# Kernel tuning notes

Measured on AMD Instinct MI355X. Metric: run time of the kernel, lower is better.

Reference implementation:

```python
import jax, jax.numpy as jnp
import numpy as np
import math

DIM = 2048; H = 16; QR = 1536; KVR = 512; DN = 128; DR = 64; DV = 128
BS = 4; S = 1024
QK_HEAD = DN + DR  # 192


def _rms(x, w, eps=1e-6):
    v = jnp.mean(x * x, axis=-1, keepdims=True)
    return w * (x * jax.lax.rsqrt(v + eps))


def _rope_cos_sin(seq_len, dim):
    inv_freq = 1.0 / (10000.0 ** (jnp.arange(0, dim, 2, dtype=jnp.float32) / dim))
    t = jnp.arange(seq_len, dtype=jnp.float32)
    freqs = jnp.einsum('s,d->sd', t, inv_freq)
    freqs = jnp.concatenate([freqs, freqs], axis=-1)  # [S, dim]
    return jnp.cos(freqs), jnp.sin(freqs)


def _rotate_half(x):
    x1, x2 = jnp.split(x, 2, axis=-1)
    return jnp.concatenate([-x2, x1], axis=-1)


def setup_inputs() -> dict:
    key = jax.random.key(0)
    ks = jax.random.split(key, 12)
    sd = 0.02
    x = jax.random.normal(ks[0], (BS, S, DIM), dtype=jnp.float32)
    # causal additive mask [b, s, t]
    i = jnp.arange(S)
    causal = jnp.where(i[:, None] >= i[None, :], 0.0, -1e9).astype(jnp.float32)
    mask = jnp.broadcast_to(causal, (BS, S, S))
    return {
        'x': x,
        'mask': mask,
        'wq_a_w': jax.random.normal(ks[1], (QR, DIM)) * sd,
        'wq_a_b': jnp.zeros((QR,), jnp.float32),
        'q_norm_w': jnp.ones((QR,), jnp.float32),
        'wq_b_w': jax.random.normal(ks[2], (H * QK_HEAD, QR)) * sd,
        'wq_b_b': jnp.zeros((H * QK_HEAD,), jnp.float32),
        'wkv_a_w': jax.random.normal(ks[3], (KVR + DR, DIM)) * sd,
        'wkv_a_b': jnp.zeros((KVR + DR,), jnp.float32),
        'kv_norm_w': jnp.ones((KVR,), jnp.float32),
        'wkv_b_w': jax.random.normal(ks[4], (H * (DN + DV), KVR)) * sd,
        'wo_w': jax.random.normal(ks[5], (DIM, H * DV)) * sd,
        'wo_b': jnp.zeros((DIM,), jnp.float32),
    }


def reference(x, mask, wq_a_w, wq_a_b, q_norm_w, wq_b_w, wq_b_b,
              wkv_a_w, wkv_a_b, kv_norm_w, wkv_b_w, wo_w, wo_b):
    bs, seq_len, _ = x.shape
    # Q low-rank path
    q = x @ wq_a_w.T + wq_a_b                     # [b,s,QR]
    q = _rms(q, q_norm_w)
    q = q @ wq_b_w.T + wq_b_b                     # [b,s,H*192]
    q = q.reshape(bs, seq_len, H, QK_HEAD)
    q_nope, q_pe = q[..., :DN], q[..., DN:]       # [b,s,h,128], [b,s,h,64]
    # compressed KV path
    kv = x @ wkv_a_w.T + wkv_a_b                  # [b,s,KVR+64]
    c, k_pe = kv[..., :KVR], kv[..., KVR:]        # [b,s,512], [b,s,64]
    # RoPE on the rope sub-dims
    cos, sin = _rope_cos_sin(seq_len, DR)         # [s,64]
    cos4 = cos[None, :, None, :]
    sin4 = sin[None, :, None, :]
    q_pe = q_pe * cos4 + _rotate_half(q_pe) * sin4
    k_pe4 = k_pe[:, :, None, :]
    k_pe = (k_pe4 * cos4 + _rotate_half(k_pe4) * sin4)[:, :, 0, :]  # [b,s,64]
    # weight absorption: wkv_b viewed [H, DN+DV, KVR]
    wkv_b = wkv_b_w.reshape(H, DN + DV, KVR)
    q_abs = jnp.einsum('bshd,hdc->bshc', q_nope, wkv_b[:, :DN])      # [b,s,h,512]
    c_n = _rms(c, kv_norm_w)                                         # [b,t,512]
    scores = (jnp.einsum('bshc,btc->bsht', q_abs, c_n)
              + jnp.einsum('bshr,btr->bsht', q_pe, k_pe)) / math.sqrt(QK_HEAD)
    scores = scores + mask[:, :, None, :]
    scores = jax.nn.softmax(scores, axis=-1)
    o = jnp.einsum('bsht,btc->bshc', scores, c_n)                    # [b,s,h,512]
    o = jnp.einsum('bshc,hdc->bshd', o, wkv_b[:, -DV:])              # [b,s,h,128]
    o = o.reshape(bs, seq_len, H * DV)
    return o @ wo_w.T + wo_b
```

## Files before the change

### kernel.cpp

```cpp
#include <hip/hip_runtime.h>


typedef __attribute__((ext_vector_type(8))) short bf16x8;
typedef __attribute__((ext_vector_type(4))) float f32x4;
typedef __attribute__((ext_vector_type(4))) int i32x4;
typedef unsigned short ushort_t;
typedef unsigned int uint32;

typedef const __attribute__((address_space(1))) void* gas_ptr;
typedef __attribute__((address_space(3))) void* las_ptr;

#define DEV __device__ __forceinline__
#define WAITVM(N) asm volatile("s_waitcnt vmcnt(" #N ")" ::: "memory")

DEV float b2f(ushort_t u) { return __uint_as_float(((uint32)u) << 16); }
DEV ushort_t f2b(float f) {
  uint32 u = __float_as_uint(f);
  return (ushort_t)((u + 0x7fffu + ((u >> 16) & 1u)) >> 16);
}
DEV uint32 pkb(float lo, float hi) { return (uint32)f2b(lo) | ((uint32)f2b(hi) << 16); }

DEV void c4seg(const float4* __restrict__ in, ushort4* __restrict__ out, int i, int n4) {
  if (i < n4) {
    float4 v = in[i];
    ushort4 o; o.x = f2b(v.x); o.y = f2b(v.y); o.z = f2b(v.z); o.w = f2b(v.w);
    out[i] = o;
  }
}
DEV void vbseg(const float* __restrict__ in, ushort_t* __restrict__ out, int i4, int dofs) {
  int c4 = i4 & 127, d = (i4 >> 7) & 127, h = i4 >> 14;
  const float4 v = *(const float4*)(in + ((long)(h * 256 + dofs + d)) * 512 + c4 * 4);
  ushort4 o; o.x = f2b(v.x); o.y = f2b(v.y); o.z = f2b(v.z); o.w = f2b(v.w);
  ((ushort4*)out)[i4] = o;
}
__global__ __launch_bounds__(256) void castall_k(
    const float* __restrict__ x, const float* __restrict__ wq_a_w,
    const float* __restrict__ wkv_a_w, const float* __restrict__ wq_b_w,
    const float* __restrict__ wo_w, const float* __restrict__ wkv_b_w,
    ushort_t* __restrict__ xb, ushort_t* __restrict__ wcomb,
    ushort_t* __restrict__ wqb, ushort_t* __restrict__ wo,
    ushort_t* __restrict__ wkvbv, ushort_t* __restrict__ wkvbn) {
  int blk = blockIdx.x, tid = threadIdx.x;
  if (blk < 8192) {
    c4seg((const float4*)x, (ushort4*)xb, blk * 256 + tid, 2097152);
  } else if (blk < 11264) {
    c4seg((const float4*)wq_a_w, (ushort4*)wcomb, (blk - 8192) * 256 + tid, 786432);
  } else if (blk < 12416) {
    c4seg((const float4*)wkv_a_w, (ushort4*)(wcomb + 1536 * 2048),
          (blk - 11264) * 256 + tid, 294912);
  } else if (blk < 17024) {
    c4seg((const float4*)wq_b_w, (ushort4*)wqb, (blk - 12416) * 256 + tid, 1179648);
  } else if (blk < 21120) {
    c4seg((const float4*)wo_w, (ushort4*)wo, (blk - 17024) * 256 + tid, 1048576);
  } else if (blk < 22144) {
    vbseg(wkv_b_w, wkvbv, (blk - 21120) * 256 + tid, 128);
  } else {
    vbseg(wkv_b_w, wkvbn, (blk - 22144) * 256 + tid, 0);
  }
}

__global__ __launch_bounds__(512) void rmskv_k(const ushort_t* __restrict__ qab,
                                               ushort_t* __restrict__ qan,
                                               const float* __restrict__ q_norm_w,
                                               const ushort_t* __restrict__ kvfb,
                                               const float* __restrict__ kv_norm_w,
                                               ushort_t* __restrict__ kcat,
                                               ushort_t* __restrict__ vtp,
                                               ushort_t* __restrict__ kabs) {
  __shared__ float sbuf[8];
  __shared__ ushort_t sh[8 * 512];
  int blk = blockIdx.x, tid = threadIdx.x;
  int wv = tid >> 6, lane = tid & 63;
  if (blk < 4096) {
    long row = blk;
    const ushort_t* p = qab + row * 1536;
    float v0 = b2f(p[tid]), v1 = b2f(p[tid + 512]), v2 = b2f(p[tid + 1024]);
    float ss = v0 * v0 + v1 * v1 + v2 * v2;
#pragma unroll
    for (int d = 1; d <= 32; d <<= 1) ss += __shfl_xor(ss, d);
    if (lane == 0) sbuf[wv] = ss;
    __syncthreads();
    float tot = 0.f;
#pragma unroll
    for (int i = 0; i < 8; ++i) tot += sbuf[i];
    float sc = rsqrtf(tot * (1.0f / 1536.0f) + 1e-6f);
    qan[row * 1536 + tid] = f2b(v0 * sc * q_norm_w[tid]);
    qan[row * 1536 + tid + 512] = f2b(v1 * sc * q_norm_w[tid + 512]);
    qan[row * 1536 + tid + 1024] = f2b(v2 * sc * q_norm_w[tid + 1024]);
  } else {
    int kb = blk - 4096;
    long row = (long)kb * 8 + wv;
    const ushort_t* p = kvfb + row * 576;
    uint4 raw = *(const uint4*)(p + lane * 8);
    const ushort_t* pr = (const ushort_t*)&raw;
    float vv[8];
#pragma unroll
    for (int j = 0; j < 8; ++j) vv[j] = b2f(pr[j]);
    float ss = 0.f;
#pragma unroll
    for (int j = 0; j < 8; ++j) ss += vv[j] * vv[j];
#pragma unroll
    for (int d = 1; d <= 32; d <<= 1) ss += __shfl_xor(ss, d);
    float sc = rsqrtf(ss * (1.0f / 512.0f) + 1e-6f);
    float4 w0 = *(const float4*)(kv_norm_w + lane * 8);
    float4 w1 = *(const float4*)(kv_norm_w + lane * 8 + 4);
    ushort_t tmp[8];
    tmp[0] = f2b(vv[0] * sc * w0.x); tmp[1] = f2b(vv[1] * sc * w0.y);
    tmp[2] = f2b(vv[2] * sc * w0.z); tmp[3] = f2b(vv[3] * sc * w0.w);
    tmp[4] = f2b(vv[4] * sc * w1.x); tmp[5] = f2b(vv[5] * sc * w1.y);
    tmp[6] = f2b(vv[6] * sc * w1.z); tmp[7] = f2b(vv[7] * sc * w1.w);
    *(uint4*)(kcat + row * 576 + lane * 8) = *(uint4*)tmp;
    *(uint4*)(sh + wv * 512 + lane * 8) = *(uint4*)tmp;
    if (lane < 32) {
      int t = (int)(row & 1023);
      float x1 = b2f(p[512 + lane]), x2 = b2f(p[544 + lane]);
      float ang = (float)t * powf(10000.0f, -(float)lane * (1.0f / 32.0f));
      float s, c; sincosf(ang, &s, &c);
      ushort_t r1 = f2b(x1 * c - x2 * s), r2 = f2b(x2 * c + x1 * s);
      kcat[row * 576 + 512 + lane] = r1;
      kcat[row * 576 + 544 + lane] = r2;
#pragma unroll
      for (int h = 0; h < 16; ++h) {
        long base = ((long)h * 4096 + row) * 192;
        kabs[base + 128 + lane] = r1;
        kabs[base + 160 + lane] = r2;
      }
    }
    __syncthreads();
    ushort_t t8[8];
#pragma unroll
    for (int j = 0; j < 8; ++j) t8[j] = sh[j * 512 + tid];
    int b = kb >> 7, tb = kb & 127;
    *(uint4*)(vtp + (((long)b * 128 + tb) * 512 + tid) * 8) = *(uint4*)t8;
  }
}

template <bool OUT_BF16>
__global__ __launch_bounds__(256) void gemm_bt_k(
    const ushort_t* __restrict__ A, int lda, long sAz,
    const ushort_t* __restrict__ B, int ldb, long sBz,
    void* __restrict__ C, int ldc, long sCz,
    const float* __restrict__ bias, float scale,
    int M, int N, int K) {
  __shared__ ushort_t As[2 * 4096];
  __shared__ ushort_t Bs[2 * 4096];
  int tid = threadIdx.x;
  int wave = tid >> 6, lane = tid & 63;
  int row0 = blockIdx.x * 128, col0 = blockIdx.y * 128;
  int z = blockIdx.z;
  const ushort_t* Az = A + (long)z * sAz;
  const ushort_t* Bz = B + (long)z * sBz;
  int wr = wave >> 1, wc = wave & 1;
  int lr = lane & 15, kq = lane >> 4;

  f32x4 acc[4][4];
#pragma unroll
  for (int m = 0; m < 4; ++m)
#pragma unroll
    for (int n = 0; n < 4; ++n) acc[m][n] = (f32x4){0.f, 0.f, 0.f, 0.f};

  auto stage = [&](int buf, int k0) {
#pragma unroll
    for (int rnd = 0; rnd < 2; ++rnd) {
      int e = rnd * 2048 + wave * 512 + lane * 8;
      int tr = e >> 5, tc = e & 31;
      int ar = row0 + tr; if (ar >= M) ar = M - 1;
      int br = col0 + tr; if (br >= N) br = N - 1;
      __builtin_amdgcn_global_load_lds((gas_ptr)(Az + (long)ar * lda + (k0 + tc)),
          (las_ptr)(As + buf * 4096 + rnd * 2048 + wave * 512), 16, 0, 0);
      __builtin_amdgcn_global_load_lds((gas_ptr)(Bz + (long)br * ldb + (k0 + tc)),
          (las_ptr)(Bs + buf * 4096 + rnd * 2048 + wave * 512), 16, 0, 0);
    }
  };

  stage(0, 0);
  int nk = K >> 5;
  for (int kt = 0; kt < nk; ++kt) {
    int cur = kt & 1;
    if (kt + 1 < nk) { stage(cur ^ 1, (kt + 1) * 32); WAITVM(4); }
    else { WAITVM(0); }
    __builtin_amdgcn_s_barrier();
    __builtin_amdgcn_sched_barrier(0);
    const ushort_t* Ac = As + cur * 4096;
    const ushort_t* Bc = Bs + cur * 4096;
    bf16x8 a[4], bb[4];
#pragma unroll
    for (int m = 0; m < 4; ++m)
      a[m] = *(const bf16x8*)(Ac + (wr * 64 + m * 16 + lr) * 32 + kq * 8);
#pragma unroll
    for (int n = 0; n < 4; ++n)
      bb[n] = *(const bf16x8*)(Bc + (wc * 64 + n * 16 + lr) * 32 + kq * 8);
#pragma unroll
    for (int m = 0; m < 4; ++m)
#pragma unroll
      for (int n = 0; n < 4; ++n)
        acc[m][n] = __builtin_amdgcn_mfma_f32_16x16x32_bf16(bb[n], a[m], acc[m][n], 0, 0, 0);
    __builtin_amdgcn_s_barrier();
  }

#pragma unroll
  for (int m = 0; m < 4; ++m) {
    int gr = row0 + wr * 64 + m * 16 + lr;
    if (gr >= M) continue;
#pragma unroll
    for (int n = 0; n < 4; ++n) {
      int cb = col0 + wc * 64 + n * 16 + kq * 4;
      if (cb >= N) continue;
      f32x4 v = acc[m][n];
#pragma unroll
      for (int r = 0; r < 4; ++r) v[r] = v[r] * scale + (bias ? bias[cb + r] : 0.f);
      long ci = (long)z * sCz + (long)gr * ldc + cb;
      if constexpr (OUT_BF16) {
        ushort4 pk; pk.x = f2b(v[0]); pk.y = f2b(v[1]); pk.z = f2b(v[2]); pk.w = f2b(v[3]);
        *(ushort4*)((ushort_t*)C + ci) = pk;
      } else {
        *(f32x4*)((float*)C + ci) = v;
      }
    }
  }
}

template <int MODE>
__global__ __launch_bounds__(256) void gemm64_k(
    const ushort_t* __restrict__ A, int lda,
    const ushort_t* __restrict__ B, int ldb,
    void* __restrict__ C, int ldc,
    const float* __restrict__ bias,
    void* __restrict__ C2, const float* __restrict__ bias2,
    int M, int N, int K) {
  __shared__ ushort_t SM[32768];
  ushort_t* As = SM;
  ushort_t* Bs = SM + 16384;
  int tid = threadIdx.x;
  int wave = tid >> 6, lane = tid & 63;
  int bid = blockIdx.y * gridDim.x + blockIdx.x;
  int nwg = gridDim.x * gridDim.y;
  int swz = (bid & 7) * (nwg >> 3) + (bid >> 3);
  int bx = swz % gridDim.x, by = swz / gridDim.x;
  int row0 = bx * 128, col0 = by * 128;
  int wr = wave >> 1, wc = wave & 1;
  int lr = lane & 15, kq = lane >> 4;
  int rsw = lr & 7;

  f32x4 acc[4][4];
#pragma unroll
  for (int m = 0; m < 4; ++m)
#pragma unroll
    for (int n = 0; n < 4; ++n) acc[m][n] = (f32x4){0.f, 0.f, 0.f, 0.f};

  auto stage = [&](int buf, int k0) {
#pragma unroll
    for (int ii = 0; ii < 4; ++ii) {
      int e = ii * 256 + tid;
      int r = e >> 3, c = e & 7;
      int scol = ((c ^ (r & 7)) << 3);
      int ar = row0 + r; if (ar >= M) ar = M - 1;
      int br = col0 + r; if (br >= N) br = N - 1;
      __builtin_amdgcn_global_load_lds((gas_ptr)(A + (long)ar * lda + k0 + scol),
          (las_ptr)(As + buf * 8192 + e * 8), 16, 0, 0);
      __builtin_amdgcn_global_load_lds((gas_ptr)(B + (long)br * ldb + k0 + scol),
          (las_ptr)(Bs + buf * 8192 + e * 8), 16, 0, 0);
    }
  };

  stage(0, 0);
  int nk = K >> 6;
  for (int kt = 0; kt < nk; ++kt) {
    int cur = kt & 1;
    if (kt + 1 < nk) { stage(cur ^ 1, (kt + 1) * 64); WAITVM(8); }
    else { WAITVM(0); }
    __builtin_amdgcn_s_barrier();
    __builtin_amdgcn_sched_barrier(0);
    const ushort_t* Ac = As + cur * 8192;
    const ushort_t* Bc = Bs + cur * 8192;
#pragma unroll
    for (int ks = 0; ks < 2; ++ks) {
      bf16x8 a[4], bb[4];
#pragma unroll
      for (int m = 0; m < 4; ++m) {
        int row = wr * 64 + m * 16 + lr;
        a[m] = *(const bf16x8*)(Ac + row * 64 + ((((ks << 2) | kq) ^ rsw) << 3));
      }
#pragma unroll
      for (int n = 0; n < 4; ++n) {
        int row = wc * 64 + n * 16 + lr;
        bb[n] = *(const bf16x8*)(Bc + row * 64 + ((((ks << 2) | kq) ^ rsw) << 3));
      }
#pragma unroll
      for (int m = 0; m < 4; ++m)
#pragma unroll
        for (int n = 0; n < 4; ++n)
          acc[m][n] = __builtin_amdgcn_mfma_f32_16x16x32_bf16(bb[n], a[m], acc[m][n], 0, 0, 0);
    }
    __builtin_amdgcn_s_barrier();
  }

  if constexpr (MODE == 0 || MODE == 1) {
    float* fs = (float*)SM;
#pragma unroll
    for (int p = 0; p < 2; ++p) {
      if (wr == p) {
#pragma unroll
        for (int m = 0; m < 4; ++m) {
#pragma unroll
          for (int n = 0; n < 4; ++n) {
            int rl = m * 16 + lr;
            int cl = wc * 64 + n * 16 + kq * 4;
            int cb = col0 + cl;
            int cbb = (cb + 3 < N) ? cb : (N - 4);
            f32x4 v = acc[m][n];
#pragma unroll
            for (int r = 0; r < 4; ++r) {
              float bv;
              if constexpr (MODE == 1)
                bv = (cbb + r < 1536) ? bias[cbb + r] : bias2[cbb + r - 1536];
              else
                bv = bias[cbb + r];
              v[r] += bv;
            }
            *(f32x4*)&fs[rl * 132 + cl] = v;
          }
        }
      }
      __syncthreads();
#pragma unroll
      for (int j = 0; j < 8; ++j) {
        int u = j * 256 + tid;
        int rl = u >> 5, off = (u & 31) << 2;
        int gr = row0 + p * 64 + rl;
        int gc = col0 + off;
        if (gr < M && gc < N) {
          f32x4 vv = *(const f32x4*)&fs[rl * 132 + off];
          if constexpr (MODE == 1) {
            ushort4 pk;
            pk.x = f2b(vv[0]); pk.y = f2b(vv[1]); pk.z = f2b(vv[2]); pk.w = f2b(vv[3]);
            if (gc < 1536) *(ushort4*)((ushort_t*)C + (long)gr * 1536 + gc) = pk;
            else           *(ushort4*)((ushort_t*)C2 + (long)gr * 576 + (gc - 1536)) = pk;
          } else {
            *(f32x4*)((float*)C + (long)gr * ldc + gc) = vv;
          }
        }
      }
      __syncthreads();
    }
  } else {
    const float RS = 0.07216878364870322f;
#pragma unroll
    for (int n = 0; n < 4; ++n) {
      int cb = col0 + wc * 64 + n * 16 + kq * 4;
      int h = cb / 192, d0 = cb - h * 192;
      ushort_t* qh = (ushort_t*)C + (long)h * 4096 * 192;
      if (d0 < 128) {
        f32x4 bv;
#pragma unroll
        for (int r = 0; r < 4; ++r) bv[r] = bias[cb + r];
#pragma unroll
        for (int m = 0; m < 4; ++m) {
          int gr = row0 + wr * 64 + m * 16 + lr;
          f32x4 v = acc[m][n];
          ushort4 pk;
          pk.x = f2b((v[0] + bv[0]) * RS); pk.y = f2b((v[1] + bv[1]) * RS);
          pk.z = f2b((v[2] + bv[2]) * RS); pk.w = f2b((v[3] + bv[3]) * RS);
          *(ushort4*)(qh + (long)gr * 192 + d0) = pk;
        }
      } else if (d0 < 160) {
        int nn = (n < 2) ? n : 0;
        f32x4 bv1, bv2, invf;
#pragma unroll
        for (int r = 0; r < 4; ++r) {
          bv1[r] = bias[cb + r]; bv2[r] = bias[cb + 32 + r];
          invf[r] = powf(10000.0f, -(float)(d0 - 128 + r) * (1.0f / 32.0f));
        }
#pragma unroll
        for (int m = 0; m < 4; ++m) {
          int gr = row0 + wr * 64 + m * 16 + lr;
          int t = gr & 1023;
          f32x4 v1 = acc[m][nn], v2 = acc[m][nn + 2];
          ushort4 p1, p2;
#pragma unroll
          for (int r = 0; r < 4; ++r) {
            float s, c; sincosf((float)t * invf[r], &s, &c);
            float x1 = v1[r] + bv1[r], x2 = v2[r] + bv2[r];
            ((ushort_t*)&p1)[r] = f2b((x1 * c - x2 * s) * RS);
            ((ushort_t*)&p2)[r] = f2b((x2 * c + x1 * s) * RS);
          }
          *(ushort4*)(qh + (long)gr * 192 + d0) = p1;
          *(ushort4*)(qh + (long)gr * 192 + d0 + 32) = p2;
        }
      }
    }
  }
}

__global__ __launch_bounds__(512, 1) void flash5_k(const ushort_t* __restrict__ qcat2,
                                                   const ushort_t* __restrict__ kabs,
                                                   const ushort_t* __restrict__ vtp,
                                                   ushort_t* __restrict__ O) {
  __shared__ __align__(16) ushort_t SMEM[2 * 6400 + 2 * 16384];

  int tid = threadIdx.x;
  int wave = tid >> 6, lane = tid & 63;
  int lr = lane & 15, kq = lane >> 4;
  int bi = blockIdx.x;
  int jz = bi >> 6;
  int qb = (jz < 4) ? jz : 11 - jz;
  int bh = bi & 63;
  int h = bh >> 2, b = bh & 3;
  int s0 = qb * 128;
  int nt = (qb + 1) * 4;

  const ushort_t* kt = kabs + ((long)h * 4096 + b * 1024) * 192;
  const ushort_t* vt = vtp + (long)b * 524288;
  const ushort_t* qp = qcat2 + ((long)(h * 4096 + b * 1024 + s0 + wave * 16 + lr)) * 192 + kq * 8;

  auto stageK = [&](int buf, int t0) {
    const ushort_t* sb = kt + (long)t0 * 192;
    ushort_t* kb = SMEM + buf * 6400;
#pragma unroll
    for (int ii = 0; ii < 2; ++ii) {
      int c = ii * 512 + tid;
      if (ii == 1 && tid >= 288) break;
      int t = (int)((unsigned)c / 25u);
      int r = c - t * 25;
      int rr = (r == 24) ? 0 : r;
      const ushort_t* src = sb + t * 192 + rr * 8;
      __builtin_amdgcn_global_load_lds((gas_ptr)src, (las_ptr)(kb + c * 8), 16, 0, 0);
    }
  };
  auto stageV = [&](int buf, int t0) {
    const ushort_t* sb = vt + (long)(t0 >> 3) * 4096;
    ushort_t* vb = SMEM + 12800 + buf * 16384;
#pragma unroll
    for (int ii = 0; ii < 4; ++ii) {
      int c0 = (ii * 8 + wave) * 64;
      const ushort_t* src = sb + (long)(c0 + lane) * 8;
      __builtin_amdgcn_global_load_lds((gas_ptr)src, (las_ptr)(vb + c0 * 8), 16, 0, 0);
    }
  };

  stageK(0, 0); stageV(0, 0);
  bf16x8 qreg[6];
#pragma unroll
  for (int st = 0; st < 6; ++st) qreg[st] = *(const bf16x8*)(qp + st * 32);

  f32x4 o[32];
#pragma unroll
  for (int v = 0; v < 32; ++v) o[v] = (f32x4){0.f, 0.f, 0.f, 0.f};
  float m_run = -1e30f, l_run = 0.f;

  int row_g = s0 + wave * 16 + lr;
  int idx_lo = (((kq & 1) << 5) + lr) << 2;
  int idx_hi = idx_lo + 64;
  bool losel = (kq < 2);

  __syncthreads();

  for (int it = 0; it < nt; ++it) {
    int cur = it & 1;
    if (it + 1 < nt) { stageK(cur ^ 1, (it + 1) * 32); stageV(cur ^ 1, (it + 1) * 32); }
    const ushort_t* Kc = SMEM + cur * 6400;
    f32x4 sv0 = (f32x4){0.f, 0.f, 0.f, 0.f}, sv1 = sv0;
    __builtin_amdgcn_s_setprio(1);
#pragma unroll
    for (int st = 0; st < 6; ++st) {
      int off = st * 32 + kq * 8;
      bf16x8 k0 = *(const bf16x8*)(Kc + lr * 200 + off);
      bf16x8 k1 = *(const bf16x8*)(Kc + (16 + lr) * 200 + off);
      sv0 = __builtin_amdgcn_mfma_f32_16x16x32_bf16(k0, qreg[st], sv0, 0, 0, 0);
      sv1 = __builtin_amdgcn_mfma_f32_16x16x32_bf16(k1, qreg[st], sv1, 0, 0, 0);
    }
    __builtin_amdgcn_s_setprio(0);
    int t0 = it * 32;
    if (t0 >= s0) {
#pragma unroll
      for (int rr = 0; rr < 4; ++rr) {
        if (t0 + kq * 4 + rr > row_g) sv0[rr] = -1e30f;
        if (t0 + 16 + kq * 4 + rr > row_g) sv1[rr] = -1e30f;
      }
    }
    float mx = fmaxf(fmaxf(fmaxf(sv0[0], sv0[1]), fmaxf(sv0[2], sv0[3])),
                     fmaxf(fmaxf(sv1[0], sv1[1]), fmaxf(sv1[2], sv1[3])));
    mx = fmaxf(mx, __shfl_xor(mx, 16));
    mx = fmaxf(mx, __shfl_xor(mx, 32));
    float mn = (mx > m_run + 8.0f) ? mx : m_run;
    float alpha = __expf(m_run - mn);
    float p0 = __expf(sv0[0] - mn), p1 = __expf(sv0[1] - mn);
    float p2 = __expf(sv0[2] - mn), p3 = __expf(sv0[3] - mn);
    float p4 = __expf(sv1[0] - mn), p5 = __expf(sv1[1] - mn);
    float p6 = __expf(sv1[2] - mn), p7 = __expf(sv1[3] - mn);
    float psum = ((p0 + p1) + (p2 + p3)) + ((p4 + p5) + (p6 + p7));
    psum += __shfl_xor(psum, 16);
    psum += __shfl_xor(psum, 32);
    l_run = l_run * alpha + psum;
    m_run = mn;
    int u0 = (int)pkb(p0, p1), u1 = (int)pkb(p2, p3);
    int u2 = (int)pkb(p4, p5), u3 = (int)pkb(p6, p7);
    int b00 = __builtin_amdgcn_ds_bpermute(idx_lo, u0);
    int b10 = __builtin_amdgcn_ds_bpermute(idx_lo, u1);
    int b20 = __builtin_amdgcn_ds_bpermute(idx_lo, u2);
    int b30 = __builtin_amdgcn_ds_bpermute(idx_lo, u3);
    int b01 = __builtin_amdgcn_ds_bpermute(idx_hi, u0);
    int b11 = __builtin_amdgcn_ds_bpermute(idx_hi, u1);
    int b21 = __builtin_amdgcn_ds_bpermute(idx_hi, u2);
    int b31 = __builtin_amdgcn_ds_bpermute(idx_hi, u3);
    i32x4 w;
    w.x = losel ? b00 : b20; w.y = losel ? b10 : b30;
    w.z = losel ? b01 : b21; w.w = losel ? b11 : b31;
    bf16x8 pa = __builtin_bit_cast(bf16x8, w);
    float a0 = __shfl(alpha, kq * 4 + 0), a1 = __shfl(alpha, kq * 4 + 1);
    float a2 = __shfl(alpha, kq * 4 + 2), a3 = __shfl(alpha, kq * 4 + 3);
    if (__any((a0 != 1.f) | (a1 != 1.f) | (a2 != 1.f) | (a3 != 1.f))) {
      f32x4 av; av[0] = a0; av[1] = a1; av[2] = a2; av[3] = a3;
#pragma unroll
      for (int v = 0; v < 32; ++v) o[v] *= av;
    }
    const ushort_t* Vc = SMEM + 12800 + cur * 16384 + (kq * 512 + lr) * 8;
    __builtin_amdgcn_s_setprio(1);
#pragma unroll
    for (int v = 0; v < 32; ++v) {
      bf16x8 bv = *(const bf16x8*)(Vc + v * 128);
      o[v] = __builtin_amdgcn_mfma_f32_16x16x32_bf16(pa, bv, o[v], 0, 0, 0);
    }
    __builtin_amdgcn_s_setprio(0);
    __syncthreads();
  }
  float l0 = __shfl(l_run, kq * 4 + 0), l1 = __shfl(l_run, kq * 4 + 1);
  float l2 = __shfl(l_run, kq * 4 + 2), l3 = __shfl(l_run, kq * 4 + 3);
  f32x4 inv; inv[0] = 1.f / l0; inv[1] = 1.f / l1; inv[2] = 1.f / l2; inv[3] = 1.f / l3;
  ushort_t* ob = O + ((long)(h * 4096 + b * 1024 + s0 + wave * 16 + kq * 4)) * 512 + lr;
#pragma unroll
  for (int rr = 0; rr < 4; ++rr) {
    ushort_t* orow = ob + (long)rr * 512;
#pragma unroll
    for (int v = 0; v < 32; ++v) orow[v * 16] = f2b(o[v][rr] * inv[rr]);
  }
}

extern "C" void kernel_launch(void* const* d_in, const int* in_sizes, int n_in,
                              void* d_out, int out_size, void* d_ws, size_t ws_size,
                              hipStream_t stream) {
  (void)in_sizes; (void)n_in;
  const float* x         = (const float*)d_in[0];
  const float* wq_a_w    = (const float*)d_in[2];
  const float* wq_a_b    = (const float*)d_in[3];
  const float* q_norm_w  = (const float*)d_in[4];
  const float* wq_b_w    = (const float*)d_in[5];
  const float* wq_b_b    = (const float*)d_in[6];
  const float* wkv_a_w   = (const float*)d_in[7];
  const float* wkv_a_b   = (const float*)d_in[8];
  const float* kv_norm_w = (const float*)d_in[9];
  const float* wkv_b_w   = (const float*)d_in[10];
  const float* wo_w      = (const float*)d_in[11];
  const float* wo_b      = (const float*)d_in[12];

  char* ws = (char*)d_ws;
  constexpr size_t OFF_XB     = 0;
  constexpr size_t OFF_WCOMB  = 16777216;
  constexpr size_t OFF_WQB    = 25427968;
  constexpr size_t OFF_QA     = 34865152;
  constexpr size_t OFF_QAN    = 60030976;
  constexpr size_t OFF_QCAT2  = 72613888;
  constexpr size_t OFF_WKVBN  = 97779712;
  constexpr size_t OFF_WKVBV  = 99876864;
  constexpr size_t OFF_WO     = 101974016;
  constexpr size_t OFF_KVF    = 110362624;
  constexpr size_t OFF_KCAT   = 119799808;
  constexpr size_t OFF_VTP    = 124518400;
  constexpr size_t OFF_KABS   = 128712704;
  constexpr size_t OFF_O      = 153878528;
  constexpr size_t OFF_O2     = 220987392;
  constexpr size_t WS_NEED    = 237764608;
  if (ws_size < WS_NEED) {
    (void)hipMemsetAsync(d_out, 0, (size_t)out_size * sizeof(float), stream);
    return;
  }

  ushort_t* xb     = (ushort_t*)(ws + OFF_XB);
  ushort_t* wcomb  = (ushort_t*)(ws + OFF_WCOMB);
  ushort_t* wqb    = (ushort_t*)(ws + OFF_WQB);
  ushort_t* qab    = (ushort_t*)(ws + OFF_QA);
  ushort_t* qan    = (ushort_t*)(ws + OFF_QAN);
  ushort_t* qcat2  = (ushort_t*)(ws + OFF_QCAT2);
  ushort_t* wkvbn  = (ushort_t*)(ws + OFF_WKVBN);
  ushort_t* wkvbv  = (ushort_t*)(ws + OFF_WKVBV);
  ushort_t* wo     = (ushort_t*)(ws + OFF_WO);
  ushort_t* kvfb   = (ushort_t*)(ws + OFF_KVF);
  ushort_t* kcat   = (ushort_t*)(ws + OFF_KCAT);
  ushort_t* vtp    = (ushort_t*)(ws + OFF_VTP);
  ushort_t* kabs   = (ushort_t*)(ws + OFF_KABS);
  ushort_t* Obuf   = (ushort_t*)(ws + OFF_O);
  ushort_t* o2     = (ushort_t*)(ws + OFF_O2);

  castall_k<<<23168, 256, 0, stream>>>(x, wq_a_w, wkv_a_w, wq_b_w, wo_w, wkv_b_w,
                                       xb, wcomb, wqb, wo, wkvbv, wkvbn);
  gemm64_k<1><<<dim3(32, 17), 256, 0, stream>>>(xb, 2048, wcomb, 2048,
      qab, 1536, wq_a_b, kvfb, wkv_a_b, 4096, 2112, 2048);
  rmskv_k<<<4608, 512, 0, stream>>>(qab, qan, q_norm_w, kvfb, kv_norm_w, kcat, vtp, kabs);
  gemm64_k<2><<<dim3(32, 24), 256, 0, stream>>>(qan, 1536, wqb, 1536,
      qcat2, 0, wq_b_b, nullptr, nullptr, 4096, 3072, 1536);
  gemm_bt_k<true><<<dim3(32, 1, 16), 256, 0, stream>>>(kcat, 576, 0,
      wkvbn, 512, (long)128 * 512, kabs, 192, (long)4096 * 192,
      nullptr, 1.f, 4096, 128, 512);
  flash5_k<<<512, 512, 0, stream>>>(qcat2, kabs, vtp, Obuf);
  gemm_bt_k<true><<<dim3(32, 1, 16), 256, 0, stream>>>(Obuf, 512, (long)4096 * 512,
      wkvbv, 512, (long)128 * 512, o2, 2048, 128, nullptr, 1.f, 4096, 128, 512);
  gemm64_k<0><<<dim3(32, 16), 256, 0, stream>>>(o2, 2048, wo, 2048,
      (float*)d_out, 2048, wo_b, nullptr, nullptr, 4096, 2048, 2048);
}
```

Measured before the change: 354.6 us.

## Split PV stage across wave pairs sharing P via LDS to halve V reads

In the flash attention kernel, the P·V product is restructured so that each pair of waves handles 32 query rows, and each wave in the pair takes half of the 512 value columns. P tiles and softmax rescale factors are exchanged through a small LDS scratch area with an added barrier, replacing the per-wave ds_bpermute shuffles. Each V fragment loaded from LDS now feeds two MFMAs instead of one, so LDS read traffic for V is halved. The cost is an extra workgroup barrier per tile and additional LDS writes and reads for P.

After: 354.6 us. Within noise of the previous version (+0.0%).

```diff
diff --git a/kernel.cpp b/kernel.cpp
--- a/kernel.cpp
+++ b/kernel.cpp
@@ -392,15 +392,18 @@
   }
 }
 
-__global__ __launch_bounds__(512, 1) void flash5_k(const ushort_t* __restrict__ qcat2,
+__global__ __launch_bounds__(512, 1) void flash8_k(const ushort_t* __restrict__ qcat2,
                                                    const ushort_t* __restrict__ kabs,
                                                    const ushort_t* __restrict__ vtp,
                                                    ushort_t* __restrict__ O) {
-  __shared__ __align__(16) ushort_t SMEM[2 * 6400 + 2 * 16384];
+  __shared__ __align__(16) ushort_t SMEM[2 * 6400 + 2 * 16384 + 128 * 40 + 256];
+  constexpr int PS_OFF = 45568;
+  float* aL = (float*)(SMEM + PS_OFF + 5120);
 
   int tid = threadIdx.x;
   int wave = tid >> 6, lane = tid & 63;
   int lr = lane & 15, kq = lane >> 4;
+  int qg = wave >> 1, vch = wave & 1;
   int bi = blockIdx.x;
   int jz = bi >> 6;
   int qb = (jz < 4) ? jz : 11 - jz;
@@ -443,15 +446,15 @@
 #pragma unroll
   for (int st = 0; st < 6; ++st) qreg[st] = *(const bf16x8*)(qp + st * 32);
 
-  f32x4 o[32];
-#pragma unroll
-  for (int v = 0; v < 32; ++v) o[v] = (f32x4){0.f, 0.f, 0.f, 0.f};
+  f32x4 oA[16], oB[16];
+#pragma unroll
+  for (int v = 0; v < 16; ++v) {
+    oA[v] = (f32x4){0.f, 0.f, 0.f, 0.f};
+    oB[v] = (f32x4){0.f, 0.f, 0.f, 0.f};
+  }
   float m_run = -1e30f, l_run = 0.f;
 
   int row_g = s0 + wave * 16 + lr;
-  int idx_lo = (((kq & 1) << 5) + lr) << 2;
-  int idx_hi = idx_lo + 64;
-  bool losel = (kq < 2);
 
   __syncthreads();
 
@@ -493,46 +496,53 @@
     psum += __shfl_xor(psum, 32);
     l_run = l_run * alpha + psum;
     m_run = mn;
-    int u0 = (int)pkb(p0, p1), u1 = (int)pkb(p2, p3);
-    int u2 = (int)pkb(p4, p5), u3 = (int)pkb(p6, p7);
-    int b00 = __builtin_amdgcn_ds_bpermute(idx_lo, u0);
-    int b10 = __builtin_amdgcn_ds_bpermute(idx_lo, u1);
-    int b20 = __builtin_amdgcn_ds_bpermute(idx_lo, u2);
-    int b30 = __builtin_amdgcn_ds_bpermute(idx_lo, u3);
-    int b01 = __builtin_amdgcn_ds_bpermute(idx_hi, u0);
-    int b11 = __builtin_amdgcn_ds_bpermute(idx_hi, u1);
-    int b21 = __builtin_amdgcn_ds_bpermute(idx_hi, u2);
-    int b31 = __builtin_amdgcn_ds_bpermute(idx_hi, u3);
-    i32x4 w;
-    w.x = losel ? b00 : b20; w.y = losel ? b10 : b30;
-    w.z = losel ? b01 : b21; w.w = losel ? b11 : b31;
-    bf16x8 pa = __builtin_bit_cast(bf16x8, w);
-    float a0 = __shfl(alpha, kq * 4 + 0), a1 = __shfl(alpha, kq * 4 + 1);
-    float a2 = __shfl(alpha, kq * 4 + 2), a3 = __shfl(alpha, kq * 4 + 3);
-    if (__any((a0 != 1.f) | (a1 != 1.f) | (a2 != 1.f) | (a3 != 1.f))) {
-      f32x4 av; av[0] = a0; av[1] = a1; av[2] = a2; av[3] = a3;
-#pragma unroll
-      for (int v = 0; v < 32; ++v) o[v] *= av;
-    }
-    const ushort_t* Vc = SMEM + 12800 + cur * 16384 + (kq * 512 + lr) * 8;
+    ushort_t* prow = SMEM + PS_OFF + (wave * 16 + lr) * 40;
+    *(uint32*)(prow + kq * 4)      = pkb(p0, p1);
+    *(uint32*)(prow + kq * 4 + 2)  = pkb(p2, p3);
+    *(uint32*)(prow + 16 + kq * 4) = pkb(p4, p5);
+    *(uint32*)(prow + 18 + kq * 4) = pkb(p6, p7);
+    if (kq == 0) aL[wave * 16 + lr] = alpha;
+    asm volatile("s_waitcnt lgkmcnt(0)" ::: "memory");
+    __builtin_amdgcn_sched_barrier(0);
+    __builtin_amdgcn_s_barrier();
+    f32x4 avA = *(const f32x4*)&aL[qg * 32 + kq * 4];
+    f32x4 avB = *(const f32x4*)&aL[qg * 32 + 16 + kq * 4];
+    bool need = (avA[0] != 1.f) | (avA[1] != 1.f) | (avA[2] != 1.f) | (avA[3] != 1.f) |
+                (avB[0] != 1.f) | (avB[1] != 1.f) | (avB[2] != 1.f) | (avB[3] != 1.f);
+    if (__any(need)) {
+#pragma unroll
+      for (int v = 0; v < 16; ++v) { oA[v] *= avA; oB[v] *= avB; }
+    }
+    bf16x8 paA = *(const bf16x8*)(SMEM + PS_OFF + (qg * 32 + lr) * 40 + kq * 8);
+    bf16x8 paB = *(const bf16x8*)(SMEM + PS_OFF + (qg * 32 + 16 + lr) * 40 + kq * 8);
+    const ushort_t* Vc = SMEM + 12800 + cur * 16384 + (kq * 512 + vch * 256 + lr) * 8;
     __builtin_amdgcn_s_setprio(1);
 #pragma unroll
-    for (int v = 0; v < 32; ++v) {
+    for (int v = 0; v < 16; ++v) {
       bf16x8 bv = *(const bf16x8*)(Vc + v * 128);
-      o[v] = __builtin_amdgcn_mfma_f32_16x16x32_bf16(pa, bv, o[v], 0, 0, 0);
+      oA[v] = __builtin_amdgcn_mfma_f32_16x16x32_bf16(paA, bv, oA[v], 0, 0, 0);
+      oB[v] = __builtin_amdgcn_mfma_f32_16x16x32_bf16(paB, bv, oB[v], 0, 0, 0);
     }
     __builtin_amdgcn_s_setprio(0);
     __syncthreads();
   }
-  float l0 = __shfl(l_run, kq * 4 + 0), l1 = __shfl(l_run, kq * 4 + 1);
-  float l2 = __shfl(l_run, kq * 4 + 2), l3 = __shfl(l_run, kq * 4 + 3);
-  f32x4 inv; inv[0] = 1.f / l0; inv[1] = 1.f / l1; inv[2] = 1.f / l2; inv[3] = 1.f / l3;
-  ushort_t* ob = O + ((long)(h * 4096 + b * 1024 + s0 + wave * 16 + kq * 4)) * 512 + lr;
+  if (kq == 0) aL[wave * 16 + lr] = l_run;
+  __syncthreads();
+  f32x4 lA = *(const f32x4*)&aL[qg * 32 + kq * 4];
+  f32x4 lB = *(const f32x4*)&aL[qg * 32 + 16 + kq * 4];
+  f32x4 invA, invB;
+#pragma unroll
+  for (int rr = 0; rr < 4; ++rr) { invA[rr] = 1.f / lA[rr]; invB[rr] = 1.f / lB[rr]; }
+  ushort_t* ob = O + ((long)(h * 4096 + b * 1024 + s0 + qg * 32 + kq * 4)) * 512 + vch * 256 + lr;
 #pragma unroll
   for (int rr = 0; rr < 4; ++rr) {
-    ushort_t* orow = ob + (long)rr * 512;
-#pragma unroll
-    for (int v = 0; v < 32; ++v) orow[v * 16] = f2b(o[v][rr] * inv[rr]);
+    ushort_t* orA = ob + (long)rr * 512;
+    ushort_t* orB = ob + (long)(16 + rr) * 512;
+#pragma unroll
+    for (int v = 0; v < 16; ++v) {
+      orA[v * 16] = f2b(oA[v][rr] * invA[rr]);
+      orB[v * 16] = f2b(oB[v][rr] * invB[rr]);
+    }
   }
 }
 
@@ -601,7 +611,7 @@
   gemm_bt_k<true><<<dim3(32, 1, 16), 256, 0, stream>>>(kcat, 576, 0,
       wkvbn, 512, (long)128 * 512, kabs, 192, (long)4096 * 192,
       nullptr, 1.f, 4096, 128, 512);
-  flash5_k<<<512, 512, 0, stream>>>(qcat2, kabs, vtp, Obuf);
+  flash8_k<<<512, 512, 0, stream>>>(qcat2, kabs, vtp, Obuf);
   gemm_bt_k<true><<<dim3(32, 1, 16), 256, 0, stream>>>(Obuf, 512, (long)4096 * 512,
       wkvbv, 512, (long)128 * 512, o2, 2048, 128, nullptr, 1.f, 4096, 128, 512);
   gemm64_k<0><<<dim3(32, 16), 256, 0, stream>>>(o2, 2048, wo, 2048,
```
